# Kernel optimization log

Measured on AMD Instinct MI355X. Metric: run time of the kernel, lower is better.

Reference implementation:

```python
import jax, jax.numpy as jnp
import numpy as np

B, H, L, D = 8, 8, 512, 512
NV = 8            # n_vars
TOP_P = 0.5
ALPHA = 0.5
EPS = 1e-10


def setup_inputs() -> dict:
    key = jax.random.key(0)
    ks = jax.random.split(key, 8)
    dh = D // H
    x = jax.random.normal(ks[0], (B, L, D), jnp.float32)
    # structural masks [L, 3, L]: S (same position across vars), T (same var block), ST (rest)
    N = L // NV
    idx = jnp.arange(L)
    kk = idx[:, None]
    S = ((idx[None, :] % N == kk % N) & (idx[None, :] != kk)).astype(jnp.float32)
    T = ((idx[None, :] >= (kk // N) * N) & (idx[None, :] < (kk // N) * N + N)).astype(jnp.float32)
    ST = 1.0 - S - T
    masks = jnp.stack([S, T, ST], axis=1)  # [L, 3, L]
    s = 0.05
    W1 = jax.random.normal(ks[1], (dh, dh), jnp.float32) * s
    b1 = jnp.zeros((dh,), jnp.float32)
    W2 = jax.random.normal(ks[2], (dh, dh), jnp.float32) * s
    b2 = jnp.zeros((dh,), jnp.float32)
    Wg = jax.random.normal(ks[3], (3, L), jnp.float32) * s   # gate: Linear(L, 3, bias=False)
    Wp = jax.random.normal(ks[4], (D, D), jnp.float32) * s   # GCN proj
    bp = jnp.zeros((D,), jnp.float32)
    return {"x": x, "masks": masks, "W1": W1, "b1": b1, "W2": W2, "b2": b2,
            "Wg": Wg, "Wp": Wp, "bp": bp}


def _forward(x, masks, W1, b1, W2, b2, Wg, Wp, bp):
    Bb, Ll, Dd = x.shape
    dh = Dd // H
    xh = x.reshape(Bb, Ll, H, dh).transpose(0, 2, 1, 3)          # [B,H,L,dh]
    q = xh @ W1.T + b1
    k = xh @ W2.T + b2
    adj = jax.nn.gelu(jnp.einsum('bhid,bhjd->bhij', q, k), approximate=False)  # [B,H,L,L]
    # mask_topk: zero out the k smallest entries per row (largest=False)
    ksm = int(ALPHA * Ll)
    thr = jnp.sort(adj, axis=-1)[..., ksm - 1:ksm]               # k-th smallest value
    adj = adj * (adj > thr).astype(adj.dtype)
    # ---- mask_moe (eval mode: clean logits) ----
    xf = adj.reshape(Bb * H, Ll, Ll)
    logits = jax.nn.softmax(xf @ Wg.T, axis=-1)                  # [BH,L,3]
    loss_dyn = -(logits * jnp.log(logits + EPS)).sum(axis=1).mean()
    order = jnp.argsort(-logits, axis=-1)                        # descending
    sorted_probs = jnp.take_along_axis(logits, order, axis=-1)
    cum = jnp.cumsum(sorted_probs, axis=-1)
    m = cum > TOP_P
    thr_idx = jnp.argmax(m.astype(jnp.int32), axis=-1)           # first expert crossing top_p
    thr_mask = jax.nn.one_hot(thr_idx, 3, dtype=jnp.bool_)
    m = m & (~thr_mask)                                          # True = dropped sorted slot
    selected = (~m).astype(jnp.float32)                          # [BH,L,3] over sorted slots
    # scatter selection back to original expert order
    top_p_mask = jnp.einsum('blj,blje->ble', selected, jax.nn.one_hot(order, 3, dtype=jnp.float32))
    sp = jnp.where(m, 0.0, sorted_probs)
    imp = sp.sum(axis=0)                                         # [L,3]
    loss_imp = jnp.var(imp, ddof=1) / (jnp.mean(imp) ** 2 + EPS)
    loss = loss_imp + 0.1 * loss_dyn
    gates = top_p_mask.reshape(Bb, H, Ll, 3)
    mask = jnp.einsum('bhli,lid->bhld', gates, masks) + jnp.eye(Ll, dtype=jnp.float32)[None, None]
    adj = adj * mask
    # ---- softmax + GCN ----
    adj = jax.nn.softmax(adj, axis=-1)
    adj = adj / jnp.clip(jnp.abs(adj).sum(axis=-1, keepdims=True), 1e-12)  # F.normalize p=1
    xp = (x @ Wp.T + bp).reshape(Bb, Ll, H, dh)                  # [B,L,H,dh]
    out = jnp.einsum('bhij,bjhd->bihd', adj, xp).reshape(Bb, Ll, Dd)
    return out, loss


def reference(x, masks, W1, b1, W2, b2, Wg, Wp, bp):
    return _forward(x, masks, W1, b1, W2, b2, Wg, Wp, bp)
```

## Files before the change

### kernel.cpp

```cpp
#include <hip/hip_runtime.h>
#include <hip/hip_bf16.h>
#include <math.h>

static constexpr int kB = 8;
static constexpr int kH = 8;
static constexpr int kL = 512;
static constexpr int kD = 512;
static constexpr int kDH = 64;
static constexpr int kBH = 64;
static constexpr int kROWS = kBH * kL;

typedef short bf16x8 __attribute__((ext_vector_type(8)));
typedef float f32x4 __attribute__((ext_vector_type(4)));

__device__ __forceinline__ ushort f2bf(float f) {
    unsigned u = __float_as_uint(f);
    unsigned r = u + 0x7fffu + ((u >> 16) & 1u);
    return (ushort)(r >> 16);
}
__device__ __forceinline__ float bf2f(ushort h) {
    return __uint_as_float((unsigned)h << 16);
}
__device__ __forceinline__ unsigned mapf(float f) {
    unsigned u = __float_as_uint(f);
    return (u & 0x80000000u) ? ~u : (u | 0x80000000u);
}
__device__ __forceinline__ float unmapf(unsigned u) {
    return (u & 0x80000000u) ? __uint_as_float(u ^ 0x80000000u)
                             : __uint_as_float(~u);
}

__device__ __forceinline__ float gelu_fast(float v) {
    float z = v * 0.70710678118654752440f;
    float az = fabsf(z);
    float t = 1.0f / (1.0f + 0.3275911f * az);
    float ex = __expf(-az * az);
    float poly = t * (0.254829592f + t * (-0.284496736f + t * (1.421413741f +
                 t * (-1.453152027f + t * 1.061405429f))));
    float erfv = 1.0f - poly * ex;
    erfv = (z < 0.0f) ? -erfv : erfv;
    return 0.5f * v * (1.0f + erfv);
}

__global__ __launch_bounds__(256) void k_qk_xp(const float* __restrict__ x,
        const float* __restrict__ W1, const float* __restrict__ b1,
        const float* __restrict__ W2, const float* __restrict__ b2,
        const float* __restrict__ Wp, const float* __restrict__ bp,
        ushort* __restrict__ qh, ushort* __restrict__ ql,
        ushort* __restrict__ kh, ushort* __restrict__ kl,
        ushort* __restrict__ xpbT) {
    __shared__ __align__(16) char smem[3 * 64 * 68 * 4];
    int tid = threadIdx.x;
    int blk = blockIdx.x;
    if (blk < 512) {
        int b = blk >> 6, h = (blk >> 3) & 7, lt = blk & 7;
        float (*xt)[68]  = (float(*)[68])smem;
        float (*w1t)[68] = (float(*)[68])(smem + 64 * 68 * 4);
        float (*w2t)[68] = (float(*)[68])(smem + 2 * 64 * 68 * 4);
        #pragma unroll
        for (int r = 0; r < 16; ++r) {
            int e = tid + r * 256;
            int rr = e >> 6, cc = e & 63;
            xt[rr][cc]  = x[(b * kL + lt * 64 + rr) * kD + h * kDH + cc];
            w1t[rr][cc] = W1[rr * 64 + cc];
            w2t[rr][cc] = W2[rr * 64 + cc];
        }
        __syncthreads();
        int ty = tid >> 4, tx = tid & 15;
        float aq[4][4] = {}, ak[4][4] = {};
        #pragma unroll 2
        for (int c = 0; c < 64; c += 4) {
            float4 av[4], wq[4], wk[4];
            #pragma unroll
            for (int a = 0; a < 4; ++a) av[a] = *(const float4*)&xt[ty * 4 + a][c];
            #pragma unroll
            for (int j = 0; j < 4; ++j) {
                wq[j] = *(const float4*)&w1t[tx + 16 * j][c];
                wk[j] = *(const float4*)&w2t[tx + 16 * j][c];
            }
            #pragma unroll
            for (int a = 0; a < 4; ++a)
                #pragma unroll
                for (int j = 0; j < 4; ++j) {
                    aq[a][j] = fmaf(av[a].x, wq[j].x, aq[a][j]);
                    aq[a][j] = fmaf(av[a].y, wq[j].y, aq[a][j]);
                    aq[a][j] = fmaf(av[a].z, wq[j].z, aq[a][j]);
                    aq[a][j] = fmaf(av[a].w, wq[j].w, aq[a][j]);
                    ak[a][j] = fmaf(av[a].x, wk[j].x, ak[a][j]);
                    ak[a][j] = fmaf(av[a].y, wk[j].y, ak[a][j]);
                    ak[a][j] = fmaf(av[a].z, wk[j].z, ak[a][j]);
                    ak[a][j] = fmaf(av[a].w, wk[j].w, ak[a][j]);
                }
        }
        #pragma unroll
        for (int a = 0; a < 4; ++a)
            #pragma unroll
            for (int j = 0; j < 4; ++j) {
                int row = lt * 64 + ty * 4 + a;
                int col = tx + 16 * j;
                int o = ((b * kH + h) * kL + row) * kDH + col;
                float qv = aq[a][j] + b1[col];
                float kv = ak[a][j] + b2[col];
                ushort qhh = f2bf(qv), khh = f2bf(kv);
                qh[o] = qhh; ql[o] = f2bf(qv - bf2f(qhh));
                kh[o] = khh; kl[o] = f2bf(kv - bf2f(khh));
            }
    } else {
        int bxp = blk - 512;
        int it = bxp >> 3, jt = bxp & 7;
        ushort (*xbs)[72] = (ushort(*)[72])smem;
        ushort (*wbs)[72] = (ushort(*)[72])(smem + 64 * 72 * 2);
        int r = tid >> 2, s = tid & 3;
        int lane = tid & 63, wave = tid >> 6;
        int wm = wave >> 1, wn = wave & 1;
        int am = wm * 32 + (lane & 15);
        int bn = wn * 32 + (lane & 15);
        int coff = (lane >> 4) * 8;
        f32x4 acc[2][2] = {};
        const float* xsrc = x + (size_t)(it * 64 + r) * kD + s * 16;
        const float* wsrc = Wp + (size_t)(jt * 64 + r) * kD + s * 16;
        for (int kt = 0; kt < 8; ++kt) {
            union { ushort u[16]; int4 v[2]; } px, pw;
            #pragma unroll
            for (int c4 = 0; c4 < 4; ++c4) {
                float4 fx = *(const float4*)(xsrc + kt * 64 + c4 * 4);
                float4 fw = *(const float4*)(wsrc + kt * 64 + c4 * 4);
                px.u[c4 * 4 + 0] = f2bf(fx.x); px.u[c4 * 4 + 1] = f2bf(fx.y);
                px.u[c4 * 4 + 2] = f2bf(fx.z); px.u[c4 * 4 + 3] = f2bf(fx.w);
                pw.u[c4 * 4 + 0] = f2bf(fw.x); pw.u[c4 * 4 + 1] = f2bf(fw.y);
                pw.u[c4 * 4 + 2] = f2bf(fw.z); pw.u[c4 * 4 + 3] = f2bf(fw.w);
            }
            __syncthreads();
            *(int4*)&xbs[r][s * 16] = px.v[0];
            *(int4*)&xbs[r][s * 16 + 8] = px.v[1];
            *(int4*)&wbs[r][s * 16] = pw.v[0];
            *(int4*)&wbs[r][s * 16 + 8] = pw.v[1];
            __syncthreads();
            #pragma unroll
            for (int kk = 0; kk < 2; ++kk) {
                bf16x8 af[2], bf[2];
                #pragma unroll
                for (int fm = 0; fm < 2; ++fm)
                    af[fm] = *(const bf16x8*)&xbs[am + fm * 16][kk * 32 + coff];
                #pragma unroll
                for (int fn = 0; fn < 2; ++fn)
                    bf[fn] = *(const bf16x8*)&wbs[bn + fn * 16][kk * 32 + coff];
                #pragma unroll
                for (int fm = 0; fm < 2; ++fm)
                    #pragma unroll
                    for (int fn = 0; fn < 2; ++fn)
                        acc[fm][fn] = __builtin_amdgcn_mfma_f32_16x16x32_bf16(
                            af[fm], bf[fn], acc[fm][fn], 0, 0, 0);
            }
        }
        #pragma unroll
        for (int fn = 0; fn < 2; ++fn) {
            int dcol = jt * 64 + wn * 32 + (lane & 15) + fn * 16;
            float bpv = bp[dcol];
            #pragma unroll
            for (int fm = 0; fm < 2; ++fm) {
                int l0 = it * 64 + wm * 32 + fm * 16 + (lane >> 4) * 4;
                union { ushort u[4]; uint2 v; } pk;
                #pragma unroll
                for (int rr = 0; rr < 4; ++rr)
                    pk.u[rr] = f2bf(acc[fm][fn][rr] + bpv);
                *(uint2*)&xpbT[(size_t)dcol * (size_t)(kB * kL) + l0] = pk.v;
            }
        }
    }
}

__global__ __launch_bounds__(256) void k_adj(const ushort* __restrict__ qh,
        const ushort* __restrict__ ql, const ushort* __restrict__ kh,
        const ushort* __restrict__ kl, float* __restrict__ adj) {
    int blk = blockIdx.x;
    int bh = blk >> 6;
    int it = (blk >> 3) & 7, jt = blk & 7;
    __shared__ ushort ah[64][72], al[64][72];
    __shared__ ushort bh_[64][72], bl[64][72];
    int tid = threadIdx.x;
    int r = tid >> 2, s = tid & 3;
    size_t aoff = (size_t)(bh * kL + it * 64 + r) * kDH + s * 16;
    size_t boff = (size_t)(bh * kL + jt * 64 + r) * kDH + s * 16;
    *(int4*)&ah[r][s * 16]  = *(const int4*)&qh[aoff];
    *(int4*)&ah[r][s * 16 + 8]  = *(const int4*)&qh[aoff + 8];
    *(int4*)&al[r][s * 16]  = *(const int4*)&ql[aoff];
    *(int4*)&al[r][s * 16 + 8]  = *(const int4*)&ql[aoff + 8];
    *(int4*)&bh_[r][s * 16] = *(const int4*)&kh[boff];
    *(int4*)&bh_[r][s * 16 + 8] = *(const int4*)&kh[boff + 8];
    *(int4*)&bl[r][s * 16]  = *(const int4*)&kl[boff];
    *(int4*)&bl[r][s * 16 + 8]  = *(const int4*)&kl[boff + 8];
    __syncthreads();
    int lane = tid & 63, wave = tid >> 6;
    int wm = wave >> 1, wn = wave & 1;
    int am = wm * 32 + (lane & 15);
    int bn = wn * 32 + (lane & 15);
    int coff = (lane >> 4) * 8;
    f32x4 acc[2][2] = {};
    #pragma unroll
    for (int kk = 0; kk < 2; ++kk) {
        bf16x8 afh[2], afl[2], bfh[2], bfl[2];
        #pragma unroll
        for (int fm = 0; fm < 2; ++fm) {
            afh[fm] = *(const bf16x8*)&ah[am + fm * 16][kk * 32 + coff];
            afl[fm] = *(const bf16x8*)&al[am + fm * 16][kk * 32 + coff];
        }
        #pragma unroll
        for (int fn = 0; fn < 2; ++fn) {
            bfh[fn] = *(const bf16x8*)&bh_[bn + fn * 16][kk * 32 + coff];
            bfl[fn] = *(const bf16x8*)&bl[bn + fn * 16][kk * 32 + coff];
        }
        #pragma unroll
        for (int fm = 0; fm < 2; ++fm)
            #pragma unroll
            for (int fn = 0; fn < 2; ++fn) {
                acc[fm][fn] = __builtin_amdgcn_mfma_f32_16x16x32_bf16(
                    afh[fm], bfh[fn], acc[fm][fn], 0, 0, 0);
                acc[fm][fn] = __builtin_amdgcn_mfma_f32_16x16x32_bf16(
                    afh[fm], bfl[fn], acc[fm][fn], 0, 0, 0);
                acc[fm][fn] = __builtin_amdgcn_mfma_f32_16x16x32_bf16(
                    afl[fm], bfh[fn], acc[fm][fn], 0, 0, 0);
            }
    }
    int mrow = it * 64 + wm * 32 + (lane >> 4) * 4;
    int ncol = jt * 64 + wn * 32 + (lane & 15);
    #pragma unroll
    for (int fm = 0; fm < 2; ++fm)
        #pragma unroll
        for (int fn = 0; fn < 2; ++fn)
            #pragma unroll
            for (int rr = 0; rr < 4; ++rr)
                adj[((size_t)bh * kL + mrow + fm * 16 + rr) * kL + ncol + fn * 16] =
                    gelu_fast(acc[fm][fn][rr]);
}

__global__ __launch_bounds__(256) void k_select(const float* __restrict__ adj,
        const float* __restrict__ Wg,
        ushort* __restrict__ adjb,
        float* __restrict__ spbuf, float* __restrict__ entbuf) {
    int tid = threadIdx.x;
    int wave = tid >> 6, lane = tid & 63;
    int row = blockIdx.x * 4 + wave;
    int i = row & (kL - 1);
    const float* arow = adj + (size_t)row * kL;
    int j0 = lane * 8;

    float v[8];
    {
        float4 a0 = *(const float4*)&arow[j0];
        float4 a1 = *(const float4*)&arow[j0 + 4];
        v[0] = a0.x; v[1] = a0.y; v[2] = a0.z; v[3] = a0.w;
        v[4] = a1.x; v[5] = a1.y; v[6] = a1.z; v[7] = a1.w;
    }
    unsigned key[8];
    #pragma unroll
    for (int t = 0; t < 8; ++t) key[t] = mapf(v[t]);

    unsigned prefix = 0;
    int cbp = 0, cin = 512;
    int bit = 31;
    int mode = 0;
    while (bit >= 1) {
        unsigned qsz = 1u << (bit - 1);
        unsigned q1 = prefix + qsz;
        unsigned q2 = prefix + 2u * qsz;
        unsigned q3 = prefix + 3u * qsz;
        int c1 = 0, c2 = 0, c3 = 0;
        #pragma unroll
        for (int t = 0; t < 8; ++t) {
            c1 += (int)__popcll(__ballot(key[t] < q1));
            c2 += (int)__popcll(__ballot(key[t] < q2));
            c3 += (int)__popcll(__ballot(key[t] < q3));
        }
        if (255 < c1)      { cin = c1 - cbp; }
        else if (255 < c2) { cin = c2 - c1;  prefix = q1; cbp = c1; }
        else if (255 < c3) { cin = c3 - c2;  prefix = q2; cbp = c2; }
        else               { cin = cin - (c3 - cbp); prefix = q3; cbp = c3; }
        bit -= 2;
        int loc = 255 - cbp;
        if (cin == 1)        { mode = 2; break; }
        if (loc == 0)        { mode = 1; break; }
        if (loc == cin - 1)  { mode = 2; break; }
    }
    float thr;
    if (mode == 0) {
        thr = unmapf(prefix);
    } else {
        unsigned width = 1u << (bit + 1);
        unsigned acc = (mode == 1) ? 0xFFFFFFFFu : 0u;
        #pragma unroll
        for (int t = 0; t < 8; ++t) {
            unsigned d = key[t] - prefix;
            bool mem = d < width;
            if (mode == 1) acc = (mem && key[t] < acc) ? key[t] : acc;
            else           acc = (mem && key[t] > acc) ? key[t] : acc;
        }
        if (mode == 1) {
            #pragma unroll
            for (int off = 1; off < 64; off <<= 1)
                acc = min(acc, (unsigned)__shfl_xor((int)acc, off));
        } else {
            #pragma unroll
            for (int off = 1; off < 64; off <<= 1)
                acc = max(acc, (unsigned)__shfl_xor((int)acc, off));
        }
        thr = unmapf(acc);
    }

    union { float4 f4[2]; float f[8]; } wg0, wg1, wg2;
    wg0.f4[0] = *(const float4*)&Wg[j0];          wg0.f4[1] = *(const float4*)&Wg[j0 + 4];
    wg1.f4[0] = *(const float4*)&Wg[kL + j0];     wg1.f4[1] = *(const float4*)&Wg[kL + j0 + 4];
    wg2.f4[0] = *(const float4*)&Wg[2 * kL + j0]; wg2.f4[1] = *(const float4*)&Wg[2 * kL + j0 + 4];
    float l0 = 0.f, l1 = 0.f, l2 = 0.f;
    #pragma unroll
    for (int t = 0; t < 8; ++t) {
        float nv = (v[t] > thr) ? v[t] : 0.0f;
        v[t] = nv;
        l0 = fmaf(nv, wg0.f[t], l0);
        l1 = fmaf(nv, wg1.f[t], l1);
        l2 = fmaf(nv, wg2.f[t], l2);
    }
    #pragma unroll
    for (int off = 1; off < 64; off <<= 1) {
        l0 += __shfl_xor(l0, off);
        l1 += __shfl_xor(l1, off);
        l2 += __shfl_xor(l2, off);
    }
    float m = fmaxf(l0, fmaxf(l1, l2));
    float e0 = __expf(l0 - m), e1 = __expf(l1 - m), e2 = __expf(l2 - m);
    float s = e0 + e1 + e2;
    float p[3] = {e0 / s, e1 / s, e2 / s};
    int o0, o1, o2;
    if (p[0] >= p[1] && p[0] >= p[2]) o0 = 0;
    else if (p[1] >= p[2]) o0 = 1;
    else o0 = 2;
    int r0 = (o0 == 0) ? 1 : 0;
    int r1 = (o0 == 2) ? 1 : 2;
    if (p[r0] >= p[r1]) { o1 = r0; o2 = r1; } else { o1 = r1; o2 = r0; }
    float sp0 = p[o0], sp1 = p[o1], sp2 = p[o2];
    float c0 = sp0, c1 = sp0 + sp1, c2 = c1 + sp2;
    bool m0 = c0 > 0.5f, m1 = c1 > 0.5f, m2 = c2 > 0.5f;
    int ti = m0 ? 0 : (m1 ? 1 : 2);
    bool mm0 = m0 && (ti != 0);
    bool mm1 = m1 && (ti != 1);
    bool mm2 = m2 && (ti != 2);
    float g[3] = {0.f, 0.f, 0.f};
    g[o0] = mm0 ? 0.f : 1.f;
    g[o1] = mm1 ? 0.f : 1.f;
    g[o2] = mm2 ? 0.f : 1.f;
    if (lane == 0) {
        spbuf[row * 3 + 0] = mm0 ? 0.f : sp0;
        spbuf[row * 3 + 1] = mm1 ? 0.f : sp1;
        spbuf[row * 3 + 2] = mm2 ? 0.f : sp2;
        entbuf[row] = p[0] * __logf(p[0] + 1e-10f) +
                      p[1] * __logf(p[1] + 1e-10f) +
                      p[2] * __logf(p[2] + 1e-10f);
    }

    int i6 = i >> 6, i63 = i & 63;
    bool inb = ((lane >> 3) == i6);
    float sel1 = inb ? (g[1] + 1.0f) : g[0];
    float sel0 = inb ? g[1] : g[2];
    int lane8 = (lane & 7) * 8;
    float e[8], ls = 0.f;
    #pragma unroll
    for (int t = 0; t < 8; ++t) {
        bool ing = (lane8 + t) == i63;
        float av = v[t] * (ing ? sel1 : sel0);
        e[t] = __expf(av);
        ls += e[t];
    }
    #pragma unroll
    for (int off = 1; off < 64; off <<= 1) ls += __shfl_xor(ls, off);
    float inv = 1.0f / ls;
    union { ushort u[8]; int4 vv; } pk;
    #pragma unroll
    for (int t = 0; t < 8; ++t) pk.u[t] = f2bf(e[t] * inv);
    *(int4*)&adjb[(size_t)row * kL + j0] = pk.vv;
}

__global__ __launch_bounds__(256) void k_out_loss1(const ushort* __restrict__ adjb,
        const ushort* __restrict__ xpbT, float* __restrict__ out,
        const float* __restrict__ spbuf, const float* __restrict__ entbuf,
        float* __restrict__ imps_buf, float* __restrict__ entpart) {
    int tid = threadIdx.x;
    int blk = blockIdx.x;
    if (blk < 512) {
        __shared__ ushort as_[64][72];
        __shared__ ushort bs_[64][72];
        int bh = blk >> 3, it = blk & 7;
        int b = bh >> 3, h = bh & 7;
        int lane = tid & 63, wave = tid >> 6;
        int wm = wave >> 1, wn = wave & 1;
        int r = tid >> 2, s = tid & 3;
        const ushort* aG = adjb + ((size_t)(bh * kL + it * 64 + r)) * kL + s * 16;
        const ushort* bG = xpbT + ((size_t)(h * kDH + r)) * (size_t)(kB * kL) + b * kL + s * 16;
        f32x4 acc[2][2] = {};
        int am = wm * 32 + (lane & 15);
        int bn = wn * 32 + (lane & 15);
        int coff = (lane >> 4) * 8;
        for (int kt = 0; kt < 8; ++kt) {
            int4 a0 = *(const int4*)(aG + kt * 64);
            int4 a1 = *(const int4*)(aG + kt * 64 + 8);
            int4 b0 = *(const int4*)(bG + kt * 64);
            int4 b1 = *(const int4*)(bG + kt * 64 + 8);
            __syncthreads();
            *(int4*)&as_[r][s * 16] = a0;
            *(int4*)&as_[r][s * 16 + 8] = a1;
            *(int4*)&bs_[r][s * 16] = b0;
            *(int4*)&bs_[r][s * 16 + 8] = b1;
            __syncthreads();
            #pragma unroll
            for (int kk = 0; kk < 2; ++kk) {
                bf16x8 af[2], bf[2];
                #pragma unroll
                for (int fm = 0; fm < 2; ++fm)
                    af[fm] = *(const bf16x8*)&as_[am + fm * 16][kk * 32 + coff];
                #pragma unroll
                for (int fn = 0; fn < 2; ++fn)
                    bf[fn] = *(const bf16x8*)&bs_[bn + fn * 16][kk * 32 + coff];
                #pragma unroll
                for (int fm = 0; fm < 2; ++fm)
                    #pragma unroll
                    for (int fn = 0; fn < 2; ++fn)
                        acc[fm][fn] = __builtin_amdgcn_mfma_f32_16x16x32_bf16(
                            af[fm], bf[fn], acc[fm][fn], 0, 0, 0);
            }
        }
        int mrow = it * 64 + wm * 32 + (lane >> 4) * 4;
        int ncol = h * kDH + wn * 32 + (lane & 15);
        #pragma unroll
        for (int fm = 0; fm < 2; ++fm)
            #pragma unroll
            for (int fn = 0; fn < 2; ++fn)
                #pragma unroll
                for (int rr = 0; rr < 4; ++rr)
                    out[((size_t)b * kL + mrow + fm * 16 + rr) * kD + ncol + fn * 16] =
                        acc[fm][fn][rr];
    } else {
        int lb = blk - 512;
        if (lb < 6) {
            int idx = lb * 256 + tid;
            float s = 0.f;
            for (int bh = 0; bh < kBH; ++bh)
                s += spbuf[bh * (kL * 3) + idx];
            imps_buf[idx] = s;
        } else {
            int eb = lb - 6;
            const float* src = entbuf + eb * 1024 + tid * 4;
            float4 v4 = *(const float4*)src;
            float s = v4.x + v4.y + v4.z + v4.w;
            __shared__ float red[256];
            red[tid] = s;
            __syncthreads();
            for (int st = 128; st > 0; st >>= 1) {
                if (tid < st) red[tid] += red[tid + st];
                __syncthreads();
            }
            if (tid == 0) entpart[eb] = red[0];
        }
    }
}

__global__ __launch_bounds__(256) void k_loss2(const float* __restrict__ imps_buf,
        const float* __restrict__ entpart, float* __restrict__ out_loss) {
    __shared__ float red[256];
    int tid = threadIdx.x;
    float im[6];
    #pragma unroll
    for (int t = 0; t < 6; ++t) im[t] = imps_buf[t * 256 + tid];
    float ms = im[0] + im[1] + im[2] + im[3] + im[4] + im[5];
    red[tid] = ms;
    __syncthreads();
    for (int st = 128; st > 0; st >>= 1) {
        if (tid < st) red[tid] += red[tid + st];
        __syncthreads();
    }
    float mean = red[0] / (float)(kL * 3);
    __syncthreads();
    float vs = 0.f;
    #pragma unroll
    for (int t = 0; t < 6; ++t) { float d = im[t] - mean; vs = fmaf(d, d, vs); }
    red[tid] = vs;
    __syncthreads();
    for (int st = 128; st > 0; st >>= 1) {
        if (tid < st) red[tid] += red[tid + st];
        __syncthreads();
    }
    float var = red[0] / (float)(kL * 3 - 1);
    __syncthreads();
    red[tid] = (tid < 32) ? entpart[tid] : 0.f;
    __syncthreads();
    for (int st = 128; st > 0; st >>= 1) {
        if (tid < st) red[tid] += red[tid + st];
        __syncthreads();
    }
    if (tid == 0) {
        float loss_imp = var / (mean * mean + 1e-10f);
        float loss_dyn = -red[0] / (float)(kBH * 3);
        out_loss[0] = loss_imp + 0.1f * loss_dyn;
    }
}

extern "C" void kernel_launch(void* const* d_in, const int* in_sizes, int n_in,
                              void* d_out, int out_size, void* d_ws, size_t ws_size,
                              hipStream_t stream) {
    const float* x     = (const float*)d_in[0];
    const float* W1    = (const float*)d_in[2];
    const float* b1    = (const float*)d_in[3];
    const float* W2    = (const float*)d_in[4];
    const float* b2    = (const float*)d_in[5];
    const float* Wg    = (const float*)d_in[6];
    const float* Wp    = (const float*)d_in[7];
    const float* bp    = (const float*)d_in[8];
    float* out = (float*)d_out;
    float* ws  = (float*)d_ws;

    float*  adj    = ws;
    ushort* qh     = (ushort*)(ws + 16777216);
    ushort* ql     = (ushort*)(ws + 17825792);
    ushort* kh     = (ushort*)(ws + 18874368);
    ushort* kl     = (ushort*)(ws + 19922944);
    ushort* adjb   = (ushort*)(ws + 16777216);
    ushort* xpbT   = (ushort*)(ws + 25165824);
    float*  spbuf  = ws + 26214400;
    float*  entbuf = ws + 26312704;
    float*  imps_b = ws + 26345472;
    float*  entprt = ws + 26347008;

    k_qk_xp<<<1024, 256, 0, stream>>>(x, W1, b1, W2, b2, Wp, bp,
                                      qh, ql, kh, kl, xpbT);
    k_adj<<<kBH * 64, 256, 0, stream>>>(qh, ql, kh, kl, adj);
    k_select<<<kROWS / 4, 256, 0, stream>>>(adj, Wg, adjb, spbuf, entbuf);
    k_out_loss1<<<550, 256, 0, stream>>>(adjb, xpbT, out, spbuf, entbuf,
                                         imps_b, entprt);
    k_loss2<<<1, 256, 0, stream>>>(imps_b, entprt, out + (size_t)kB * kL * kD);
}
```

Baseline: 102.3 us.

## Use split-bf16 MFMA for Q/K projection and process two rows per wave in select

The Q/K projection moves from scalar fp32 FMA loops to MFMA bf16 instructions, using a hi/lo bf16 split with three products to keep accuracy near fp32. Each wave computes either Q or K for a 64x32 tile, with weights converted straight into registers. Separately, k_select now handles two rows per wave and launches half as many blocks, loading the gate weights once per two rows. The split adds conversion work and a small precision change in exchange for matrix-core throughput.

Result: no change. 103.8 us (+1.5%).

```diff
diff --git a/kernel.cpp b/kernel.cpp
--- a/kernel.cpp
+++ b/kernel.cpp
@@ -49,61 +49,94 @@
         ushort* __restrict__ qh, ushort* __restrict__ ql,
         ushort* __restrict__ kh, ushort* __restrict__ kl,
         ushort* __restrict__ xpbT) {
-    __shared__ __align__(16) char smem[3 * 64 * 68 * 4];
+    __shared__ __align__(16) char smem[2 * 64 * 72 * 2];
     int tid = threadIdx.x;
     int blk = blockIdx.x;
+    int lane = tid & 63, wave = tid >> 6;
     if (blk < 512) {
         int b = blk >> 6, h = (blk >> 3) & 7, lt = blk & 7;
-        float (*xt)[68]  = (float(*)[68])smem;
-        float (*w1t)[68] = (float(*)[68])(smem + 64 * 68 * 4);
-        float (*w2t)[68] = (float(*)[68])(smem + 2 * 64 * 68 * 4);
-        #pragma unroll
-        for (int r = 0; r < 16; ++r) {
-            int e = tid + r * 256;
-            int rr = e >> 6, cc = e & 63;
-            xt[rr][cc]  = x[(b * kL + lt * 64 + rr) * kD + h * kDH + cc];
-            w1t[rr][cc] = W1[rr * 64 + cc];
-            w2t[rr][cc] = W2[rr * 64 + cc];
+        ushort (*xhi)[72] = (ushort(*)[72])smem;
+        ushort (*xlo)[72] = (ushort(*)[72])(smem + 64 * 72 * 2);
+        {
+            int r = tid >> 2, s = tid & 3;
+            const float* src = x + (size_t)(b * kL + lt * 64 + r) * kD + h * kDH + s * 16;
+            union { ushort u[16]; int4 v[2]; } ph, pl;
+            #pragma unroll
+            for (int c4 = 0; c4 < 4; ++c4) {
+                float4 f = *(const float4*)(src + c4 * 4);
+                float fv[4] = {f.x, f.y, f.z, f.w};
+                #pragma unroll
+                for (int t = 0; t < 4; ++t) {
+                    ushort hh = f2bf(fv[t]);
+                    ph.u[c4 * 4 + t] = hh;
+                    pl.u[c4 * 4 + t] = f2bf(fv[t] - bf2f(hh));
+                }
+            }
+            *(int4*)&xhi[r][s * 16] = ph.v[0];
+            *(int4*)&xhi[r][s * 16 + 8] = ph.v[1];
+            *(int4*)&xlo[r][s * 16] = pl.v[0];
+            *(int4*)&xlo[r][s * 16 + 8] = pl.v[1];
+        }
+        int wq = wave >> 1, wn = wave & 1;
+        const float* Wm = wq ? W2 : W1;
+        const float* bias = wq ? b2 : b1;
+        int coff = (lane >> 4) * 8;
+        bf16x8 bh8[2][2], bl8[2][2];
+        #pragma unroll
+        for (int fn = 0; fn < 2; ++fn) {
+            int browg = wn * 32 + fn * 16 + (lane & 15);
+            #pragma unroll
+            for (int kk = 0; kk < 2; ++kk) {
+                const float* wsrc = Wm + browg * 64 + kk * 32 + coff;
+                float4 f0 = *(const float4*)(wsrc);
+                float4 f1 = *(const float4*)(wsrc + 4);
+                float fv[8] = {f0.x, f0.y, f0.z, f0.w, f1.x, f1.y, f1.z, f1.w};
+                union { ushort u[8]; bf16x8 v; } uh, ul;
+                #pragma unroll
+                for (int t = 0; t < 8; ++t) {
+                    ushort hh = f2bf(fv[t]);
+                    uh.u[t] = hh;
+                    ul.u[t] = f2bf(fv[t] - bf2f(hh));
+                }
+                bh8[fn][kk] = uh.v;
+                bl8[fn][kk] = ul.v;
+            }
         }
         __syncthreads();
-        int ty = tid >> 4, tx = tid & 15;
-        float aq[4][4] = {}, ak[4][4] = {};
-        #pragma unroll 2
-        for (int c = 0; c < 64; c += 4) {
-            float4 av[4], wq[4], wk[4];
-            #pragma unroll
-            for (int a = 0; a < 4; ++a) av[a] = *(const float4*)&xt[ty * 4 + a][c];
-            #pragma unroll
-            for (int j = 0; j < 4; ++j) {
-                wq[j] = *(const float4*)&w1t[tx + 16 * j][c];
-                wk[j] = *(const float4*)&w2t[tx + 16 * j][c];
-            }
-            #pragma unroll
-            for (int a = 0; a < 4; ++a)
-                #pragma unroll
-                for (int j = 0; j < 4; ++j) {
-                    aq[a][j] = fmaf(av[a].x, wq[j].x, aq[a][j]);
-                    aq[a][j] = fmaf(av[a].y, wq[j].y, aq[a][j]);
-                    aq[a][j] = fmaf(av[a].z, wq[j].z, aq[a][j]);
-                    aq[a][j] = fmaf(av[a].w, wq[j].w, aq[a][j]);
-                    ak[a][j] = fmaf(av[a].x, wk[j].x, ak[a][j]);
-                    ak[a][j] = fmaf(av[a].y, wk[j].y, ak[a][j]);
-                    ak[a][j] = fmaf(av[a].z, wk[j].z, ak[a][j]);
-                    ak[a][j] = fmaf(av[a].w, wk[j].w, ak[a][j]);
+        f32x4 acc[4][2] = {};
+        #pragma unroll
+        for (int kk = 0; kk < 2; ++kk)
+            #pragma unroll
+            for (int fm = 0; fm < 4; ++fm) {
+                bf16x8 ah8 = *(const bf16x8*)&xhi[fm * 16 + (lane & 15)][kk * 32 + coff];
+                bf16x8 al8 = *(const bf16x8*)&xlo[fm * 16 + (lane & 15)][kk * 32 + coff];
+                #pragma unroll
+                for (int fn = 0; fn < 2; ++fn) {
+                    acc[fm][fn] = __builtin_amdgcn_mfma_f32_16x16x32_bf16(
+                        ah8, bh8[fn][kk], acc[fm][fn], 0, 0, 0);
+                    acc[fm][fn] = __builtin_amdgcn_mfma_f32_16x16x32_bf16(
+                        ah8, bl8[fn][kk], acc[fm][fn], 0, 0, 0);
+                    acc[fm][fn] = __builtin_amdgcn_mfma_f32_16x16x32_bf16(
+                        al8, bh8[fn][kk], acc[fm][fn], 0, 0, 0);
                 }
-        }
-        #pragma unroll
-        for (int a = 0; a < 4; ++a)
-            #pragma unroll
-            for (int j = 0; j < 4; ++j) {
-                int row = lt * 64 + ty * 4 + a;
-                int col = tx + 16 * j;
-                int o = ((b * kH + h) * kL + row) * kDH + col;
-                float qv = aq[a][j] + b1[col];
-                float kv = ak[a][j] + b2[col];
-                ushort qhh = f2bf(qv), khh = f2bf(kv);
-                qh[o] = qhh; ql[o] = f2bf(qv - bf2f(qhh));
-                kh[o] = khh; kl[o] = f2bf(kv - bf2f(khh));
+            }
+        ushort* dh = wq ? kh : qh;
+        ushort* dl = wq ? kl : ql;
+        #pragma unroll
+        for (int fm = 0; fm < 4; ++fm)
+            #pragma unroll
+            for (int fn = 0; fn < 2; ++fn) {
+                int col = wn * 32 + fn * 16 + (lane & 15);
+                float bv = bias[col];
+                #pragma unroll
+                for (int rr = 0; rr < 4; ++rr) {
+                    int row = lt * 64 + fm * 16 + (lane >> 4) * 4 + rr;
+                    int o = ((b * kH + h) * kL + row) * kDH + col;
+                    float val = acc[fm][fn][rr] + bv;
+                    ushort hh = f2bf(val);
+                    dh[o] = hh;
+                    dl[o] = f2bf(val - bf2f(hh));
+                }
             }
     } else {
         int bxp = blk - 512;
@@ -111,7 +144,6 @@
         ushort (*xbs)[72] = (ushort(*)[72])smem;
         ushort (*wbs)[72] = (ushort(*)[72])(smem + 64 * 72 * 2);
         int r = tid >> 2, s = tid & 3;
-        int lane = tid & 63, wave = tid >> 6;
         int wm = wave >> 1, wn = wave & 1;
         int am = wm * 32 + (lane & 15);
         int bn = wn * 32 + (lane & 15);
@@ -240,143 +272,147 @@
         float* __restrict__ spbuf, float* __restrict__ entbuf) {
     int tid = threadIdx.x;
     int wave = tid >> 6, lane = tid & 63;
-    int row = blockIdx.x * 4 + wave;
-    int i = row & (kL - 1);
-    const float* arow = adj + (size_t)row * kL;
     int j0 = lane * 8;
-
-    float v[8];
-    {
-        float4 a0 = *(const float4*)&arow[j0];
-        float4 a1 = *(const float4*)&arow[j0 + 4];
-        v[0] = a0.x; v[1] = a0.y; v[2] = a0.z; v[3] = a0.w;
-        v[4] = a1.x; v[5] = a1.y; v[6] = a1.z; v[7] = a1.w;
-    }
-    unsigned key[8];
-    #pragma unroll
-    for (int t = 0; t < 8; ++t) key[t] = mapf(v[t]);
-
-    unsigned prefix = 0;
-    int cbp = 0, cin = 512;
-    int bit = 31;
-    int mode = 0;
-    while (bit >= 1) {
-        unsigned qsz = 1u << (bit - 1);
-        unsigned q1 = prefix + qsz;
-        unsigned q2 = prefix + 2u * qsz;
-        unsigned q3 = prefix + 3u * qsz;
-        int c1 = 0, c2 = 0, c3 = 0;
-        #pragma unroll
-        for (int t = 0; t < 8; ++t) {
-            c1 += (int)__popcll(__ballot(key[t] < q1));
-            c2 += (int)__popcll(__ballot(key[t] < q2));
-            c3 += (int)__popcll(__ballot(key[t] < q3));
-        }
-        if (255 < c1)      { cin = c1 - cbp; }
-        else if (255 < c2) { cin = c2 - c1;  prefix = q1; cbp = c1; }
-        else if (255 < c3) { cin = c3 - c2;  prefix = q2; cbp = c2; }
-        else               { cin = cin - (c3 - cbp); prefix = q3; cbp = c3; }
-        bit -= 2;
-        int loc = 255 - cbp;
-        if (cin == 1)        { mode = 2; break; }
-        if (loc == 0)        { mode = 1; break; }
-        if (loc == cin - 1)  { mode = 2; break; }
-    }
-    float thr;
-    if (mode == 0) {
-        thr = unmapf(prefix);
-    } else {
-        unsigned width = 1u << (bit + 1);
-        unsigned acc = (mode == 1) ? 0xFFFFFFFFu : 0u;
-        #pragma unroll
-        for (int t = 0; t < 8; ++t) {
-            unsigned d = key[t] - prefix;
-            bool mem = d < width;
-            if (mode == 1) acc = (mem && key[t] < acc) ? key[t] : acc;
-            else           acc = (mem && key[t] > acc) ? key[t] : acc;
-        }
-        if (mode == 1) {
-            #pragma unroll
-            for (int off = 1; off < 64; off <<= 1)
-                acc = min(acc, (unsigned)__shfl_xor((int)acc, off));
-        } else {
-            #pragma unroll
-            for (int off = 1; off < 64; off <<= 1)
-                acc = max(acc, (unsigned)__shfl_xor((int)acc, off));
-        }
-        thr = unmapf(acc);
-    }
 
     union { float4 f4[2]; float f[8]; } wg0, wg1, wg2;
     wg0.f4[0] = *(const float4*)&Wg[j0];          wg0.f4[1] = *(const float4*)&Wg[j0 + 4];
     wg1.f4[0] = *(const float4*)&Wg[kL + j0];     wg1.f4[1] = *(const float4*)&Wg[kL + j0 + 4];
     wg2.f4[0] = *(const float4*)&Wg[2 * kL + j0]; wg2.f4[1] = *(const float4*)&Wg[2 * kL + j0 + 4];
-    float l0 = 0.f, l1 = 0.f, l2 = 0.f;
-    #pragma unroll
-    for (int t = 0; t < 8; ++t) {
-        float nv = (v[t] > thr) ? v[t] : 0.0f;
-        v[t] = nv;
-        l0 = fmaf(nv, wg0.f[t], l0);
-        l1 = fmaf(nv, wg1.f[t], l1);
-        l2 = fmaf(nv, wg2.f[t], l2);
-    }
-    #pragma unroll
-    for (int off = 1; off < 64; off <<= 1) {
-        l0 += __shfl_xor(l0, off);
-        l1 += __shfl_xor(l1, off);
-        l2 += __shfl_xor(l2, off);
-    }
-    float m = fmaxf(l0, fmaxf(l1, l2));
-    float e0 = __expf(l0 - m), e1 = __expf(l1 - m), e2 = __expf(l2 - m);
-    float s = e0 + e1 + e2;
-    float p[3] = {e0 / s, e1 / s, e2 / s};
-    int o0, o1, o2;
-    if (p[0] >= p[1] && p[0] >= p[2]) o0 = 0;
-    else if (p[1] >= p[2]) o0 = 1;
-    else o0 = 2;
-    int r0 = (o0 == 0) ? 1 : 0;
-    int r1 = (o0 == 2) ? 1 : 2;
-    if (p[r0] >= p[r1]) { o1 = r0; o2 = r1; } else { o1 = r1; o2 = r0; }
-    float sp0 = p[o0], sp1 = p[o1], sp2 = p[o2];
-    float c0 = sp0, c1 = sp0 + sp1, c2 = c1 + sp2;
-    bool m0 = c0 > 0.5f, m1 = c1 > 0.5f, m2 = c2 > 0.5f;
-    int ti = m0 ? 0 : (m1 ? 1 : 2);
-    bool mm0 = m0 && (ti != 0);
-    bool mm1 = m1 && (ti != 1);
-    bool mm2 = m2 && (ti != 2);
-    float g[3] = {0.f, 0.f, 0.f};
-    g[o0] = mm0 ? 0.f : 1.f;
-    g[o1] = mm1 ? 0.f : 1.f;
-    g[o2] = mm2 ? 0.f : 1.f;
-    if (lane == 0) {
-        spbuf[row * 3 + 0] = mm0 ? 0.f : sp0;
-        spbuf[row * 3 + 1] = mm1 ? 0.f : sp1;
-        spbuf[row * 3 + 2] = mm2 ? 0.f : sp2;
-        entbuf[row] = p[0] * __logf(p[0] + 1e-10f) +
-                      p[1] * __logf(p[1] + 1e-10f) +
-                      p[2] * __logf(p[2] + 1e-10f);
-    }
-
-    int i6 = i >> 6, i63 = i & 63;
-    bool inb = ((lane >> 3) == i6);
-    float sel1 = inb ? (g[1] + 1.0f) : g[0];
-    float sel0 = inb ? g[1] : g[2];
-    int lane8 = (lane & 7) * 8;
-    float e[8], ls = 0.f;
-    #pragma unroll
-    for (int t = 0; t < 8; ++t) {
-        bool ing = (lane8 + t) == i63;
-        float av = v[t] * (ing ? sel1 : sel0);
-        e[t] = __expf(av);
-        ls += e[t];
-    }
-    #pragma unroll
-    for (int off = 1; off < 64; off <<= 1) ls += __shfl_xor(ls, off);
-    float inv = 1.0f / ls;
-    union { ushort u[8]; int4 vv; } pk;
-    #pragma unroll
-    for (int t = 0; t < 8; ++t) pk.u[t] = f2bf(e[t] * inv);
-    *(int4*)&adjb[(size_t)row * kL + j0] = pk.vv;
+
+    for (int rl = 0; rl < 2; ++rl) {
+        int row = blockIdx.x * 8 + wave * 2 + rl;
+        int i = row & (kL - 1);
+        const float* arow = adj + (size_t)row * kL;
+
+        float v[8];
+        {
+            float4 a0 = *(const float4*)&arow[j0];
+            float4 a1 = *(const float4*)&arow[j0 + 4];
+            v[0] = a0.x; v[1] = a0.y; v[2] = a0.z; v[3] = a0.w;
+            v[4] = a1.x; v[5] = a1.y; v[6] = a1.z; v[7] = a1.w;
+        }
+        unsigned key[8];
+        #pragma unroll
+        for (int t = 0; t < 8; ++t) key[t] = mapf(v[t]);
+
+        unsigned prefix = 0;
+        int cbp = 0, cin = 512;
+        int bit = 31;
+        int mode = 0;
+        while (bit >= 1) {
+            unsigned qsz = 1u << (bit - 1);
+            unsigned q1 = prefix + qsz;
+            unsigned q2 = prefix + 2u * qsz;
+            unsigned q3 = prefix + 3u * qsz;
+            int c1 = 0, c2 = 0, c3 = 0;
+            #pragma unroll
+            for (int t = 0; t < 8; ++t) {
+                c1 += (int)__popcll(__ballot(key[t] < q1));
+                c2 += (int)__popcll(__ballot(key[t] < q2));
+                c3 += (int)__popcll(__ballot(key[t] < q3));
+            }
+            if (255 < c1)      { cin = c1 - cbp; }
+            else if (255 < c2) { cin = c2 - c1;  prefix = q1; cbp = c1; }
+            else if (255 < c3) { cin = c3 - c2;  prefix = q2; cbp = c2; }
+            else               { cin = cin - (c3 - cbp); prefix = q3; cbp = c3; }
+            bit -= 2;
+            int loc = 255 - cbp;
+            if (cin == 1)        { mode = 2; break; }
+            if (loc == 0)        { mode = 1; break; }
+            if (loc == cin - 1)  { mode = 2; break; }
+        }
+        float thr;
+        if (mode == 0) {
+            thr = unmapf(prefix);
+        } else {
+            unsigned width = 1u << (bit + 1);
+            unsigned acc = (mode == 1) ? 0xFFFFFFFFu : 0u;
+            #pragma unroll
+            for (int t = 0; t < 8; ++t) {
+                unsigned d = key[t] - prefix;
+                bool mem = d < width;
+                if (mode == 1) acc = (mem && key[t] < acc) ? key[t] : acc;
+                else           acc = (mem && key[t] > acc) ? key[t] : acc;
+            }
+            if (mode == 1) {
+                #pragma unroll
+                for (int off = 1; off < 64; off <<= 1)
+                    acc = min(acc, (unsigned)__shfl_xor((int)acc, off));
+            } else {
+                #pragma unroll
+                for (int off = 1; off < 64; off <<= 1)
+                    acc = max(acc, (unsigned)__shfl_xor((int)acc, off));
+            }
+            thr = unmapf(acc);
+        }
+
+        float l0 = 0.f, l1 = 0.f, l2 = 0.f;
+        #pragma unroll
+        for (int t = 0; t < 8; ++t) {
+            float nv = (v[t] > thr) ? v[t] : 0.0f;
+            v[t] = nv;
+            l0 = fmaf(nv, wg0.f[t], l0);
+            l1 = fmaf(nv, wg1.f[t], l1);
+            l2 = fmaf(nv, wg2.f[t], l2);
+        }
+        #pragma unroll
+        for (int off = 1; off < 64; off <<= 1) {
+            l0 += __shfl_xor(l0, off);
+            l1 += __shfl_xor(l1, off);
+            l2 += __shfl_xor(l2, off);
+        }
+        float m = fmaxf(l0, fmaxf(l1, l2));
+        float e0 = __expf(l0 - m), e1 = __expf(l1 - m), e2 = __expf(l2 - m);
+        float s = e0 + e1 + e2;
+        float p[3] = {e0 / s, e1 / s, e2 / s};
+        int o0, o1, o2;
+        if (p[0] >= p[1] && p[0] >= p[2]) o0 = 0;
+        else if (p[1] >= p[2]) o0 = 1;
+        else o0 = 2;
+        int r0 = (o0 == 0) ? 1 : 0;
+        int r1 = (o0 == 2) ? 1 : 2;
+        if (p[r0] >= p[r1]) { o1 = r0; o2 = r1; } else { o1 = r1; o2 = r0; }
+        float sp0 = p[o0], sp1 = p[o1], sp2 = p[o2];
+        float c0 = sp0, c1 = sp0 + sp1, c2 = c1 + sp2;
+        bool m0 = c0 > 0.5f, m1 = c1 > 0.5f, m2 = c2 > 0.5f;
+        int ti = m0 ? 0 : (m1 ? 1 : 2);
+        bool mm0 = m0 && (ti != 0);
+        bool mm1 = m1 && (ti != 1);
+        bool mm2 = m2 && (ti != 2);
+        float g[3] = {0.f, 0.f, 0.f};
+        g[o0] = mm0 ? 0.f : 1.f;
+        g[o1] = mm1 ? 0.f : 1.f;
+        g[o2] = mm2 ? 0.f : 1.f;
+        if (lane == 0) {
+            spbuf[row * 3 + 0] = mm0 ? 0.f : sp0;
+            spbuf[row * 3 + 1] = mm1 ? 0.f : sp1;
+            spbuf[row * 3 + 2] = mm2 ? 0.f : sp2;
+            entbuf[row] = p[0] * __logf(p[0] + 1e-10f) +
+                          p[1] * __logf(p[1] + 1e-10f) +
+                          p[2] * __logf(p[2] + 1e-10f);
+        }
+
+        int i6 = i >> 6, i63 = i & 63;
+        bool inb = ((lane >> 3) == i6);
+        float sel1 = inb ? (g[1] + 1.0f) : g[0];
+        float sel0 = inb ? g[1] : g[2];
+        int lane8 = (lane & 7) * 8;
+        float e[8], ls = 0.f;
+        #pragma unroll
+        for (int t = 0; t < 8; ++t) {
+            bool ing = (lane8 + t) == i63;
+            float av = v[t] * (ing ? sel1 : sel0);
+            e[t] = __expf(av);
+            ls += e[t];
+        }
+        #pragma unroll
+        for (int off = 1; off < 64; off <<= 1) ls += __shfl_xor(ls, off);
+        float inv = 1.0f / ls;
+        union { ushort u[8]; int4 vv; } pk;
+        #pragma unroll
+        for (int t = 0; t < 8; ++t) pk.u[t] = f2bf(e[t] * inv);
+        *(int4*)&adjb[(size_t)row * kL + j0] = pk.vv;
+    }
 }
 
 __global__ __launch_bounds__(256) void k_out_loss1(const ushort* __restrict__ adjb,
@@ -531,7 +567,7 @@
     k_qk_xp<<<1024, 256, 0, stream>>>(x, W1, b1, W2, b2, Wp, bp,
                                       qh, ql, kh, kl, xpbT);
     k_adj<<<kBH * 64, 256, 0, stream>>>(qh, ql, kh, kl, adj);
-    k_select<<<kROWS / 4, 256, 0, stream>>>(adj, Wg, adjb, spbuf, entbuf);
+    k_select<<<kROWS / 8, 256, 0, stream>>>(adj, Wg, adjb, spbuf, entbuf);
     k_out_loss1<<<550, 256, 0, stream>>>(adjb, xpbT, out, spbuf, entbuf,
                                          imps_b, entprt);
     k_loss2<<<1, 256, 0, stream>>>(imps_b, entprt, out + (size_t)kB * kL * kD);
```
